# Kernel optimization log

Measured on AMD Instinct MI355X. Metric: run time of the kernel, lower is better.

Reference implementation:

```python
import jax, jax.numpy as jnp
import numpy as np
import math

B, N, D, H = 4, 2048, 1024, 16
DH = D // H  # dim per head
OUT = 1024

def setup_inputs() -> dict:
    key0 = jax.random.key(0)
    ks = jax.random.split(key0, 12)
    s = 1.0 / math.sqrt(D)
    return {
        "key": jax.random.normal(ks[0], (B, N, D), jnp.float32),
        "value": jax.random.normal(ks[1], (B, N, D), jnp.float32),
        "query": jax.random.normal(ks[2], (B, N, D), jnp.float32),
        "Wk": jax.random.normal(ks[3], (D, D), jnp.float32) * s,
        "bk": jax.random.normal(ks[4], (D,), jnp.float32) * 0.01,
        "Wv": jax.random.normal(ks[5], (D, D), jnp.float32) * s,
        "bv": jax.random.normal(ks[6], (D,), jnp.float32) * 0.01,
        "Wq": jax.random.normal(ks[7], (D, D), jnp.float32) * s,
        "bq": jax.random.normal(ks[8], (D,), jnp.float32) * 0.01,
        "Wo": jax.random.normal(ks[9], (D, OUT), jnp.float32) * s,
        "bo": jax.random.normal(ks[10], (OUT,), jnp.float32) * 0.01,
    }

def reference(key, value, query, Wk, bk, Wv, bv, Wq, bq, Wo, bo):
    scale = math.sqrt(DH)
    k = (key @ Wk + bk).reshape(B, N, H, DH).transpose(0, 2, 1, 3)    # [B,H,N,DH]
    v = (value @ Wv + bv).reshape(B, N, H, DH).transpose(0, 2, 1, 3)
    q = ((query @ Wq + bq) / scale).reshape(B, N, H, DH).transpose(0, 2, 1, 3)
    scores = jnp.einsum('bhqd,bhkd->bhqk', q, k).astype(jnp.float32)  # [B,H,N,N]
    attn = jax.nn.softmax(scores, axis=-1).astype(q.dtype)
    # dropout p=0.0 (eval / identity)
    ctx = jnp.einsum('bhqk,bhkd->bhqd', attn, v)                      # [B,H,N,DH]
    ctx = ctx.transpose(0, 2, 1, 3).reshape(B, N, D)
    out = ctx @ Wo + bo                                               # [B,N,OUT]
    return out
```

## Files before the change

kernel.cpp:

```cpp
#include <hip/hip_runtime.h>
#include <hip/hip_bf16.h>
#include <stdint.h>

#define BB 4
#define NN 2048
#define DD 1024
#define HH 16
#define DHH 64
#define MM (BB*NN)

typedef unsigned short u16;
typedef unsigned int u32;
typedef __bf16 bf16x8_t __attribute__((ext_vector_type(8)));
typedef float f32x4_t __attribute__((ext_vector_type(4)));
typedef float f32x16_t __attribute__((ext_vector_type(16)));

__device__ inline u16 f2b(float f) {
    __hip_bfloat16 h = __float2bfloat16(f);
    return *(u16*)&h;
}

__device__ inline u32 pack2(float lo, float hi) {
    __hip_bfloat162 h2 = __float22bfloat162_rn(make_float2(lo, hi));
    return *(u32*)&h2;
}

__device__ inline void gload16(const void* g, void* l) {
    __builtin_amdgcn_global_load_lds(
        (const __attribute__((address_space(1))) void*)g,
        (__attribute__((address_space(3))) void*)l, 16, 0, 0);
}

__global__ void cvt_kernel(const float* __restrict__ in, u16* __restrict__ out) {
    int i = (blockIdx.x * 256 + threadIdx.x) * 4;
    float4 v = *(const float4*)(in + i);
    ushort4 o;
    o.x = f2b(v.x); o.y = f2b(v.y); o.z = f2b(v.z); o.w = f2b(v.w);
    *(ushort4*)(out + i) = o;
}

__global__ void wtrans_kernel(const float* __restrict__ W0, const float* __restrict__ W1,
                              const float* __restrict__ W2, const float* __restrict__ W3,
                              u16* __restrict__ out_base) {
    int z = blockIdx.z;
    const float* W = (z == 0) ? W0 : (z == 1) ? W1 : (z == 2) ? W2 : W3;
    u16* o = out_base + (size_t)z * DD * DD;
    __shared__ float tile[64][65];
    int t = threadIdx.x;
    int r0 = t >> 6;
    int c = t & 63;
    int kb = blockIdx.x, nb = blockIdx.y;
#pragma unroll
    for (int i = 0; i < 16; ++i) {
        int r = i * 4 + r0;
        tile[r][c] = W[(size_t)(kb * 64 + r) * DD + nb * 64 + c];
    }
    __syncthreads();
#pragma unroll
    for (int i = 0; i < 16; ++i) {
        int r = i * 4 + r0;
        o[(size_t)(nb * 64 + r) * DD + kb * 64 + c] = f2b(tile[c][r]);
    }
}

__global__ void vtrans_kernel(const u16* __restrict__ in, u16* __restrict__ out) {
    __shared__ u16 tile[64][65];
    const int t = threadIdx.x;
    const int r0 = t >> 6;
    const int c = t & 63;
    const int nt = blockIdx.x;
    const int bh = blockIdx.y;
    const int b = bh >> 4, h = bh & 15;
    const u16* src = in + ((size_t)(b * 2048 + nt * 64)) * DD + h * 64;
#pragma unroll
    for (int i = 0; i < 16; ++i) {
        int r = i * 4 + r0;
        tile[r][c] = src[(size_t)r * DD + c];
    }
    __syncthreads();
    u16* dst = out + ((size_t)bh * 64) * NN + nt * 64;
#pragma unroll
    for (int i = 0; i < 16; ++i) {
        int r = i * 4 + r0;
        dst[(size_t)r * NN + c] = tile[c][r];
    }
}

template<int OUT_F32>
__global__ __launch_bounds__(256, 2)
void gemm_bt(const u16* __restrict__ A, const u16* __restrict__ Bt,
             const float* __restrict__ bias, void* __restrict__ Cout, float scale) {
    __shared__ u16 As[128 * 64];
    __shared__ u16 Bs[128 * 64];
    const int t = threadIdx.x;
    const int w = t >> 6, l = t & 63;
    const int wm = w >> 1, wn = w & 1;
    const int g = l >> 4, c = l & 15;
    const int bm = blockIdx.x, bn = blockIdx.y;

    const f32x4_t vzero = {0.f, 0.f, 0.f, 0.f};
    f32x4_t acc[4][4];
#pragma unroll
    for (int m = 0; m < 4; ++m)
#pragma unroll
        for (int n = 0; n < 4; ++n) acc[m][n] = vzero;

    const int srow = l >> 3;
    const int scol = ((l & 7) ^ srow) << 3;
    const int sa = (l & 7) << 4;

    for (int ks = 0; ks < 16; ++ks) {
#pragma unroll
        for (int i = 0; i < 4; ++i) {
            int chunk = w * 4 + i;
            int row = chunk * 8 + srow;
            const u16* ga = A + (size_t)(bm * 128 + row) * DD + ks * 64 + scol;
            gload16(ga, As + chunk * 512);
            const u16* gb = Bt + (size_t)(bn * 128 + row) * DD + ks * 64 + scol;
            gload16(gb, Bs + chunk * 512);
        }
        __syncthreads();

        bf16x8_t af[4][2], bfr[4][2];
#pragma unroll
        for (int m = 0; m < 4; ++m) {
            int rowa = wm * 64 + m * 16 + c;
#pragma unroll
            for (int kk = 0; kk < 2; ++kk)
                af[m][kk] = *(const bf16x8_t*)&As[rowa * 64 + (((kk * 64 + g * 16) ^ sa) >> 1)];
        }
#pragma unroll
        for (int n = 0; n < 4; ++n) {
            int rowb = wn * 64 + n * 16 + c;
#pragma unroll
            for (int kk = 0; kk < 2; ++kk)
                bfr[n][kk] = *(const bf16x8_t*)&Bs[rowb * 64 + (((kk * 64 + g * 16) ^ sa) >> 1)];
        }
#pragma unroll
        for (int kk = 0; kk < 2; ++kk)
#pragma unroll
            for (int m = 0; m < 4; ++m)
#pragma unroll
                for (int n = 0; n < 4; ++n)
                    acc[m][n] = __builtin_amdgcn_mfma_f32_16x16x32_bf16(
                        af[m][kk], bfr[n][kk], acc[m][n], 0, 0, 0);
        __syncthreads();
    }

#pragma unroll
    for (int n = 0; n < 4; ++n) {
        int col = bn * 128 + wn * 64 + n * 16 + c;
        float bv = bias[col];
#pragma unroll
        for (int m = 0; m < 4; ++m) {
            int row = bm * 128 + wm * 64 + m * 16 + g * 4;
#pragma unroll
            for (int j = 0; j < 4; ++j) {
                float v = (acc[m][n][j] + bv) * scale;
                if (OUT_F32)
                    ((float*)Cout)[(size_t)(row + j) * DD + col] = v;
                else
                    ((u16*)Cout)[(size_t)(row + j) * DD + col] = f2b(v);
            }
        }
    }
}

__global__ __launch_bounds__(256, 2)
void attn32_kernel(const u16* __restrict__ qb, const u16* __restrict__ kb,
                   const u16* __restrict__ vt, u16* __restrict__ ctx) {
    __shared__ u16 Kt[4][64 * 64];
    __shared__ u16 Vs[4][64 * 64];
    const int t = threadIdx.x;
    const int w = t >> 6, l = t & 63;
    const int hl = l >> 5, l31 = l & 31, l7 = l & 7, l3 = l >> 3;

    const int f = blockIdx.y * 8 + blockIdx.x;
    const int wg = (f & 7) * 64 + (f >> 3);
    const int qt = wg & 7, bh = wg >> 3;
    const int b = bh >> 4, h = bh & 15;
    const int hoff = h * DHH;
    const size_t kv0 = (size_t)b * NN;
    const size_t vt0 = (size_t)bh * DHH;

    const size_t qrow_base = (size_t)(b * NN + qt * 256 + w * 64);
    bf16x8_t qf[2][4];
#pragma unroll
    for (int qm = 0; qm < 2; ++qm)
#pragma unroll
        for (int dks = 0; dks < 4; ++dks)
            qf[qm][dks] = *(const bf16x8_t*)&qb[(qrow_base + qm * 32 + l31) * DD +
                                                hoff + dks * 16 + hl * 8];

    f32x16_t z16;
#pragma unroll
    for (int r = 0; r < 16; ++r) z16[r] = 0.f;

    f32x16_t accO[2][2];
#pragma unroll
    for (int qm = 0; qm < 2; ++qm)
#pragma unroll
        for (int dt = 0; dt < 2; ++dt) accO[qm][dt] = z16;
    f32x16_t lacc16[2];
    lacc16[0] = z16; lacc16[1] = z16;

    const int scol2 = (l7 ^ l3) << 3;
    const u16* kp[2];
    const u16* vp[2];
#pragma unroll
    for (int i = 0; i < 2; ++i) {
        const int ch = w * 2 + i, r = ch * 8 + l3, rr = (r >> 2) & 3;
        const int pr = (rr == 1 || rr == 2) ? (r ^ 12) : r;
        kp[i] = kb + (kv0 + pr) * DD + hoff + scol2;
        vp[i] = vt + (vt0 + r) * NN + scol2;
    }

#define STAGE(S_)                                                            \
    do {                                                                     \
        _Pragma("unroll")                                                    \
        for (int i_ = 0; i_ < 2; ++i_) {                                     \
            gload16(kp[i_], &Kt[S_][(w * 2 + i_) * 512]);                    \
            gload16(vp[i_], &Vs[S_][(w * 2 + i_) * 512]);                    \
        }                                                                    \
        _Pragma("unroll")                                                    \
        for (int i_ = 0; i_ < 2; ++i_) { kp[i_] += 64 * DD; vp[i_] += 64; }  \
    } while (0)

    STAGE(0);
    STAGE(1);
    STAGE(2);

#pragma unroll 1
    for (int kt = 0; kt < NN / 64; ++kt) {
        const int cur = kt & 3;
        if (kt < NN / 64 - 3) {
            STAGE((kt + 3) & 3);
            asm volatile("s_waitcnt vmcnt(12)" ::: "memory");
        } else if (kt == NN / 64 - 3) {
            asm volatile("s_waitcnt vmcnt(8)" ::: "memory");
        } else if (kt == NN / 64 - 2) {
            asm volatile("s_waitcnt vmcnt(4)" ::: "memory");
        } else {
            asm volatile("s_waitcnt vmcnt(0)" ::: "memory");
        }
        __builtin_amdgcn_s_barrier();
        asm volatile("" ::: "memory");

        const char* Kc = (const char*)Kt[cur];
        const char* Vc = (const char*)Vs[cur];

        bf16x8_t kf[2][4];
#pragma unroll
        for (int kt32 = 0; kt32 < 2; ++kt32)
#pragma unroll
            for (int dks = 0; dks < 4; ++dks)
                kf[kt32][dks] = *(const bf16x8_t*)(Kc + (kt32 * 32 + l31) * 128 +
                                                   ((dks * 32 + hl * 16) ^ (l7 << 4)));

        f32x16_t accS[2][2];
        __builtin_amdgcn_s_setprio(1);
#pragma unroll
        for (int qm = 0; qm < 2; ++qm)
#pragma unroll
            for (int kt32 = 0; kt32 < 2; ++kt32) {
                accS[qm][kt32] = __builtin_amdgcn_mfma_f32_32x32x16_bf16(
                    kf[kt32][0], qf[qm][0], z16, 0, 0, 0);
#pragma unroll
                for (int dks = 1; dks < 4; ++dks)
                    accS[qm][kt32] = __builtin_amdgcn_mfma_f32_32x32x16_bf16(
                        kf[kt32][dks], qf[qm][dks], accS[qm][kt32], 0, 0, 0);
            }
        __builtin_amdgcn_s_setprio(0);

#pragma unroll
        for (int qm = 0; qm < 2; ++qm) {
#pragma unroll
            for (int kt32 = 0; kt32 < 2; ++kt32)
#pragma unroll
                for (int r = 0; r < 16; ++r)
                    accS[qm][kt32][r] = __builtin_amdgcn_exp2f(accS[qm][kt32][r]);
            lacc16[qm] += accS[qm][0] + accS[qm][1];
        }

        bf16x8_t vf[4][2];
#pragma unroll
        for (int pm = 0; pm < 4; ++pm)
#pragma unroll
            for (int dt = 0; dt < 2; ++dt)
                vf[pm][dt] = *(const bf16x8_t*)(Vc + (dt * 32 + l31) * 128 +
                                                ((pm * 32 + hl * 16) ^ (l7 << 4)));

        __builtin_amdgcn_s_setprio(1);
#pragma unroll
        for (int qm = 0; qm < 2; ++qm)
#pragma unroll
            for (int pm = 0; pm < 4; ++pm) {
                const int kt32 = pm >> 1, half = pm & 1;
                union { u32 u[4]; bf16x8_t v; } pu;
#pragma unroll
                for (int j2 = 0; j2 < 4; ++j2)
                    pu.u[j2] = pack2(accS[qm][kt32][half * 8 + 2 * j2],
                                     accS[qm][kt32][half * 8 + 2 * j2 + 1]);
#pragma unroll
                for (int dt = 0; dt < 2; ++dt)
                    accO[qm][dt] = __builtin_amdgcn_mfma_f32_32x32x16_bf16(
                        vf[pm][dt], pu.v, accO[qm][dt], 0, 0, 0);
            }
        __builtin_amdgcn_s_setprio(0);

        asm volatile("" ::: "memory");
        __builtin_amdgcn_s_barrier();
        asm volatile("" ::: "memory");
    }
#undef STAGE

#pragma unroll
    for (int qm = 0; qm < 2; ++qm) {
        float s8[8];
#pragma unroll
        for (int r = 0; r < 8; ++r) s8[r] = lacc16[qm][r] + lacc16[qm][r + 8];
#pragma unroll
        for (int sl = 4; sl >= 1; sl >>= 1)
#pragma unroll
            for (int r = 0; r < sl; ++r) s8[r] += s8[r + sl];
        float rsum = s8[0] + __shfl_xor(s8[0], 32);
        const float rl = 1.0f / rsum;
        const size_t qrow = qrow_base + qm * 32 + l31;
#pragma unroll
        for (int dt = 0; dt < 2; ++dt)
#pragma unroll
            for (int m = 0; m < 4; ++m) {
                ushort4 o;
                o.x = f2b(accO[qm][dt][4 * m + 0] * rl);
                o.y = f2b(accO[qm][dt][4 * m + 1] * rl);
                o.z = f2b(accO[qm][dt][4 * m + 2] * rl);
                o.w = f2b(accO[qm][dt][4 * m + 3] * rl);
                *(ushort4*)&ctx[qrow * DD + hoff + dt * 32 + m * 8 + hl * 4] = o;
            }
    }
}

extern "C" void kernel_launch(void* const* d_in, const int* in_sizes, int n_in,
                              void* d_out, int out_size, void* d_ws, size_t ws_size,
                              hipStream_t stream) {
    (void)in_sizes; (void)n_in; (void)out_size; (void)ws_size;
    const float* key   = (const float*)d_in[0];
    const float* value = (const float*)d_in[1];
    const float* query = (const float*)d_in[2];
    const float* Wk = (const float*)d_in[3];
    const float* bk = (const float*)d_in[4];
    const float* Wv = (const float*)d_in[5];
    const float* bv = (const float*)d_in[6];
    const float* Wq = (const float*)d_in[7];
    const float* bq = (const float*)d_in[8];
    const float* Wo = (const float*)d_in[9];
    const float* bo = (const float*)d_in[10];

    char* ws = (char*)d_ws;
    const size_t MB = 1024 * 1024;
    u16* qbuf = (u16*)(ws + 0 * MB);
    u16* kbuf = (u16*)(ws + 16 * MB);
    u16* vbuf = (u16*)(ws + 32 * MB);
    u16* WtK  = (u16*)(ws + 48 * MB);
    u16* WtV  = (u16*)(ws + 50 * MB);
    u16* WtQ  = (u16*)(ws + 52 * MB);
    u16* WtO  = (u16*)(ws + 54 * MB);
    u16* xb   = (u16*)(ws + 56 * MB);

    const int nelem = MM * DD;
    const int cvt_blocks = nelem / (256 * 4);

    wtrans_kernel<<<dim3(16, 16, 4), 256, 0, stream>>>(Wk, Wv, Wq, Wo, WtK);

    cvt_kernel<<<cvt_blocks, 256, 0, stream>>>(value, xb);
    gemm_bt<0><<<dim3(64, 8), 256, 0, stream>>>(xb, WtV, bv, vbuf, 1.0f);
    cvt_kernel<<<cvt_blocks, 256, 0, stream>>>(key, xb);
    gemm_bt<0><<<dim3(64, 8), 256, 0, stream>>>(xb, WtK, bk, kbuf, 1.0f);
    cvt_kernel<<<cvt_blocks, 256, 0, stream>>>(query, xb);
    gemm_bt<0><<<dim3(64, 8), 256, 0, stream>>>(xb, WtQ, bq, qbuf, 0.125f * 1.4426950408889634f);

    u16* VT = xb;
    vtrans_kernel<<<dim3(32, 64), 256, 0, stream>>>(vbuf, VT);

    u16* ctx = vbuf;
    attn32_kernel<<<dim3(8, 64), 256, 0, stream>>>(qbuf, kbuf, VT, ctx);

    gemm_bt<1><<<dim3(64, 8), 256, 0, stream>>>(ctx, WtO, bo, d_out, 1.0f);
}
```

Before: 208.9 us.

## Double-buffer GEMM LDS tiles and compute V projection directly transposed

The GEMM now double-buffers its A/B tiles in LDS, issuing the next stage's global loads before computing the current one. It waits with explicit vmcnt counts and raw barriers, and raises wave priority around the MFMA block. The V projection is computed as WtV times x^T per batch, using a row bias and a z-dimension grid, so it writes V already transposed and the separate vtrans kernel is removed. The cost is doubled LDS per block (64 KB), which may limit occupancy, plus a batched output layout that is harder to follow.

```diff
diff --git a/kernel.cpp b/kernel.cpp
--- a/kernel.cpp
+++ b/kernel.cpp
@@ -63,40 +63,20 @@
     }
 }
 
-__global__ void vtrans_kernel(const u16* __restrict__ in, u16* __restrict__ out) {
-    __shared__ u16 tile[64][65];
-    const int t = threadIdx.x;
-    const int r0 = t >> 6;
-    const int c = t & 63;
-    const int nt = blockIdx.x;
-    const int bh = blockIdx.y;
-    const int b = bh >> 4, h = bh & 15;
-    const u16* src = in + ((size_t)(b * 2048 + nt * 64)) * DD + h * 64;
-#pragma unroll
-    for (int i = 0; i < 16; ++i) {
-        int r = i * 4 + r0;
-        tile[r][c] = src[(size_t)r * DD + c];
-    }
-    __syncthreads();
-    u16* dst = out + ((size_t)bh * 64) * NN + nt * 64;
-#pragma unroll
-    for (int i = 0; i < 16; ++i) {
-        int r = i * 4 + r0;
-        dst[(size_t)r * NN + c] = tile[c][r];
-    }
-}
-
-template<int OUT_F32>
+template<int OUT_F32, int BIAS_ROW>
 __global__ __launch_bounds__(256, 2)
 void gemm_bt(const u16* __restrict__ A, const u16* __restrict__ Bt,
-             const float* __restrict__ bias, void* __restrict__ Cout, float scale) {
-    __shared__ u16 As[128 * 64];
-    __shared__ u16 Bs[128 * 64];
+             const float* __restrict__ bias, void* __restrict__ Cout, float scale,
+             size_t a_z, size_t bt_z, size_t c_z, int ldc) {
+    __shared__ u16 As[2][128 * 64];
+    __shared__ u16 Bs[2][128 * 64];
     const int t = threadIdx.x;
     const int w = t >> 6, l = t & 63;
     const int wm = w >> 1, wn = w & 1;
     const int g = l >> 4, c = l & 15;
-    const int bm = blockIdx.x, bn = blockIdx.y;
+    const int bm = blockIdx.x, bn = blockIdx.y, z = blockIdx.z;
+    A += (size_t)z * a_z;
+    Bt += (size_t)z * bt_z;
 
     const f32x4_t vzero = {0.f, 0.f, 0.f, 0.f};
     f32x4_t acc[4][4];
@@ -109,17 +89,38 @@
     const int scol = ((l & 7) ^ srow) << 3;
     const int sa = (l & 7) << 4;
 
+    const u16* ap[4];
+    const u16* bp[4];
+#pragma unroll
+    for (int i = 0; i < 4; ++i) {
+        const int chunk = w * 4 + i, row = chunk * 8 + srow;
+        ap[i] = A + (size_t)(bm * 128 + row) * DD + scol;
+        bp[i] = Bt + (size_t)(bn * 128 + row) * DD + scol;
+    }
+
+#define GSTAGE(buf_)                                                         \
+    do {                                                                     \
+        _Pragma("unroll")                                                    \
+        for (int i_ = 0; i_ < 4; ++i_) {                                     \
+            gload16(ap[i_], &As[buf_][(w * 4 + i_) * 512]);                  \
+            gload16(bp[i_], &Bs[buf_][(w * 4 + i_) * 512]);                  \
+            ap[i_] += 64; bp[i_] += 64;                                      \
+        }                                                                    \
+    } while (0)
+
+    GSTAGE(0);
+
+#pragma unroll 1
     for (int ks = 0; ks < 16; ++ks) {
-#pragma unroll
-        for (int i = 0; i < 4; ++i) {
-            int chunk = w * 4 + i;
-            int row = chunk * 8 + srow;
-            const u16* ga = A + (size_t)(bm * 128 + row) * DD + ks * 64 + scol;
-            gload16(ga, As + chunk * 512);
-            const u16* gb = Bt + (size_t)(bn * 128 + row) * DD + ks * 64 + scol;
-            gload16(gb, Bs + chunk * 512);
-        }
-        __syncthreads();
+        const int cur = ks & 1;
+        if (ks < 15) {
+            GSTAGE(cur ^ 1);
+            asm volatile("s_waitcnt vmcnt(8)" ::: "memory");
+        } else {
+            asm volatile("s_waitcnt vmcnt(0)" ::: "memory");
+        }
+        __builtin_amdgcn_s_barrier();
+        asm volatile("" ::: "memory");
 
         bf16x8_t af[4][2], bfr[4][2];
 #pragma unroll
@@ -127,15 +128,16 @@
             int rowa = wm * 64 + m * 16 + c;
 #pragma unroll
             for (int kk = 0; kk < 2; ++kk)
-                af[m][kk] = *(const bf16x8_t*)&As[rowa * 64 + (((kk * 64 + g * 16) ^ sa) >> 1)];
+                af[m][kk] = *(const bf16x8_t*)&As[cur][rowa * 64 + (((kk * 64 + g * 16) ^ sa) >> 1)];
         }
 #pragma unroll
         for (int n = 0; n < 4; ++n) {
             int rowb = wn * 64 + n * 16 + c;
 #pragma unroll
             for (int kk = 0; kk < 2; ++kk)
-                bfr[n][kk] = *(const bf16x8_t*)&Bs[rowb * 64 + (((kk * 64 + g * 16) ^ sa) >> 1)];
-        }
+                bfr[n][kk] = *(const bf16x8_t*)&Bs[cur][rowb * 64 + (((kk * 64 + g * 16) ^ sa) >> 1)];
+        }
+        __builtin_amdgcn_s_setprio(1);
 #pragma unroll
         for (int kk = 0; kk < 2; ++kk)
 #pragma unroll
@@ -144,23 +146,32 @@
                 for (int n = 0; n < 4; ++n)
                     acc[m][n] = __builtin_amdgcn_mfma_f32_16x16x32_bf16(
                         af[m][kk], bfr[n][kk], acc[m][n], 0, 0, 0);
-        __syncthreads();
-    }
-
+        __builtin_amdgcn_s_setprio(0);
+
+        asm volatile("" ::: "memory");
+        __builtin_amdgcn_s_barrier();
+        asm volatile("" ::: "memory");
+    }
+#undef GSTAGE
+
+    char* Cz = (char*)Cout + (size_t)z * c_z * (OUT_F32 ? 4 : 2);
 #pragma unroll
     for (int n = 0; n < 4; ++n) {
         int col = bn * 128 + wn * 64 + n * 16 + c;
-        float bv = bias[col];
+        float bcol = BIAS_ROW ? 0.f : bias[col];
 #pragma unroll
         for (int m = 0; m < 4; ++m) {
             int row = bm * 128 + wm * 64 + m * 16 + g * 4;
+            float4 brow;
+            if (BIAS_ROW) brow = *(const float4*)&bias[row];
 #pragma unroll
             for (int j = 0; j < 4; ++j) {
+                float bv = BIAS_ROW ? ((const float*)&brow)[j] : bcol;
                 float v = (acc[m][n][j] + bv) * scale;
                 if (OUT_F32)
-                    ((float*)Cout)[(size_t)(row + j) * DD + col] = v;
+                    ((float*)Cz)[(size_t)(row + j) * ldc + col] = v;
                 else
-                    ((u16*)Cout)[(size_t)(row + j) * DD + col] = f2b(v);
+                    ((u16*)Cz)[(size_t)(row + j) * ldc + col] = f2b(v);
             }
         }
     }
@@ -360,12 +371,12 @@
     const size_t MB = 1024 * 1024;
     u16* qbuf = (u16*)(ws + 0 * MB);
     u16* kbuf = (u16*)(ws + 16 * MB);
-    u16* vbuf = (u16*)(ws + 32 * MB);
+    u16* xb   = (u16*)(ws + 32 * MB);
     u16* WtK  = (u16*)(ws + 48 * MB);
     u16* WtV  = (u16*)(ws + 50 * MB);
     u16* WtQ  = (u16*)(ws + 52 * MB);
     u16* WtO  = (u16*)(ws + 54 * MB);
-    u16* xb   = (u16*)(ws + 56 * MB);
+    u16* VT   = (u16*)(ws + 56 * MB);
 
     const int nelem = MM * DD;
     const int cvt_blocks = nelem / (256 * 4);
@@ -373,17 +384,18 @@
     wtrans_kernel<<<dim3(16, 16, 4), 256, 0, stream>>>(Wk, Wv, Wq, Wo, WtK);
 
     cvt_kernel<<<cvt_blocks, 256, 0, stream>>>(value, xb);
-    gemm_bt<0><<<dim3(64, 8), 256, 0, stream>>>(xb, WtV, bv, vbuf, 1.0f);
+    gemm_bt<0, 1><<<dim3(8, 16, 4), 256, 0, stream>>>(
+        WtV, xb, bv, VT, 1.0f, 0, (size_t)2048 * DD, (size_t)1024 * 2048, 2048);
     cvt_kernel<<<cvt_blocks, 256, 0, stream>>>(key, xb);
-    gemm_bt<0><<<dim3(64, 8), 256, 0, stream>>>(xb, WtK, bk, kbuf, 1.0f);
+    gemm_bt<0, 0><<<dim3(64, 8, 1), 256, 0, stream>>>(
+        xb, WtK, bk, kbuf, 1.0f, 0, 0, 0, DD);
     cvt_kernel<<<cvt_blocks, 256, 0, stream>>>(query, xb);
-    gemm_bt<0><<<dim3(64, 8), 256, 0, stream>>>(xb, WtQ, bq, qbuf, 0.125f * 1.4426950408889634f);
-
-    u16* VT = xb;
-    vtrans_kernel<<<dim3(32, 64), 256, 0, stream>>>(vbuf, VT);
-
-    u16* ctx = vbuf;
+    gemm_bt<0, 0><<<dim3(64, 8, 1), 256, 0, stream>>>(
+        xb, WtQ, bq, qbuf, 0.125f * 1.4426950408889634f, 0, 0, 0, DD);
+
+    u16* ctx = xb;
     attn32_kernel<<<dim3(8, 64), 256, 0, stream>>>(qbuf, kbuf, VT, ctx);
 
-    gemm_bt<1><<<dim3(64, 8), 256, 0, stream>>>(ctx, WtO, bo, d_out, 1.0f);
-}
+    gemm_bt<1, 0><<<dim3(64, 8, 1), 256, 0, stream>>>(
+        ctx, WtO, bo, d_out, 1.0f, 0, 0, 0, DD);
+}
```

New measurement: 206.1 us. No clear change (-1.3%).
